# Optimization experiments

Measured on AMD Instinct MI355X. Metric: run time of the kernel, lower is better.

The kernel has to match this reference:

```python
import jax, jax.numpy as jnp
import numpy as np

FP8_MAX = 448.0  # max normal of float8_e4m3fn (TE fwd format)
EPS = 1e-12


def _fp8_quant_dequant(t):
    """Per-tensor amax scaling -> cast to e4m3 -> dequant back to f32.
    Mirrors TE's per-tensor scaling recipe (scale = FP8_MAX / amax)."""
    amax = jnp.max(jnp.abs(t))
    scale = FP8_MAX / jnp.maximum(amax, EPS)
    q = jnp.clip(t * scale, -FP8_MAX, FP8_MAX).astype(jnp.float8_e4m3fn)
    return q.astype(jnp.float32) / scale


def setup_inputs() -> dict:
    key = jax.random.key(0)
    k1, k2, k3 = jax.random.split(key, 3)
    tokens, d_in, d_out = 8192, 4096, 4096
    x = jax.random.normal(k1, (tokens, d_in), dtype=jnp.float32)
    # kaiming_uniform_(a=sqrt(5)) -> U(-bound, bound), bound = sqrt(6/((1+a^2)*fan_in)) = 1/sqrt(fan_in)
    bound = 1.0 / np.sqrt(d_in)
    weight = jax.random.uniform(k2, (d_out, d_in), dtype=jnp.float32, minval=-bound, maxval=bound)
    bias = jnp.zeros((d_out,), dtype=jnp.float32) + 0.01 * jax.random.normal(k3, (d_out,), dtype=jnp.float32)
    return {"x": x, "weight": weight, "bias": bias}


def reference(x, weight, bias):
    # fp8 quant/dequant of activations and weights, then GEMM + bias
    xq = _fp8_quant_dequant(x)            # [T, Din]
    wq = _fp8_quant_dequant(weight)       # [Dout, Din]
    out = jnp.einsum("ti,oi->to", xq, wq) # [T, Dout]
    return out + bias[None, :]
```

## Files before the change

kernel.cpp:

```cpp
#include <hip/hip_runtime.h>
#include <stdint.h>

#define M_DIM 8192
#define N_DIM 4096
#define K_DIM 4096

typedef float f32x4 __attribute__((ext_vector_type(4)));
typedef int   i32x4 __attribute__((ext_vector_type(4)));
typedef int   i32x8 __attribute__((ext_vector_type(8)));

__global__ __launch_bounds__(256) void amax2_kernel(const float* __restrict__ x,
                                                    const float* __restrict__ wgt,
                                                    unsigned int* __restrict__ ws_u) {
    const int which = blockIdx.y;
    const float4* p = (const float4*)(which ? wgt : x);
    const int n4 = (which ? N_DIM : M_DIM) * (K_DIM / 4);
    int tid = blockIdx.x * blockDim.x + threadIdx.x;
    int stride = gridDim.x * blockDim.x;
    float m = 0.0f;
    for (int i = tid; i < n4; i += stride) {
        float4 v = p[i];
        m = fmaxf(m, fmaxf(fmaxf(fabsf(v.x), fabsf(v.y)),
                           fmaxf(fabsf(v.z), fabsf(v.w))));
    }
#pragma unroll
    for (int off = 32; off > 0; off >>= 1)
        m = fmaxf(m, __shfl_down(m, off, 64));
    __shared__ float sm[4];
    if ((threadIdx.x & 63) == 0) sm[threadIdx.x >> 6] = m;
    __syncthreads();
    if (threadIdx.x == 0) {
        m = fmaxf(fmaxf(sm[0], sm[1]), fmaxf(sm[2], sm[3]));
        atomicMax(ws_u + which, __float_as_uint(m));
    }
}

__global__ __launch_bounds__(256) void quant2_kernel(const float* __restrict__ x,
                                                     const float* __restrict__ wgt,
                                                     unsigned int* __restrict__ xq,
                                                     unsigned int* __restrict__ wq,
                                                     const unsigned int* __restrict__ ws_u) {
    const int which = blockIdx.y;
    const float4* p = (const float4*)(which ? wgt : x);
    unsigned int* outp = which ? wq : xq;
    const int n4 = (which ? N_DIM : M_DIM) * (K_DIM / 4);
    float amax = fmaxf(__uint_as_float(ws_u[which]), 1e-12f);
    float scale = 448.0f / amax;
    int tid = blockIdx.x * blockDim.x + threadIdx.x;
    int stride = gridDim.x * blockDim.x;
    for (int i = tid; i < n4; i += stride) {
        float4 v = p[i];
        float a = fminf(fmaxf(v.x * scale, -448.0f), 448.0f);
        float b = fminf(fmaxf(v.y * scale, -448.0f), 448.0f);
        float c = fminf(fmaxf(v.z * scale, -448.0f), 448.0f);
        float d = fminf(fmaxf(v.w * scale, -448.0f), 448.0f);
        int w = __builtin_amdgcn_cvt_pk_fp8_f32(a, b, 0, false);
        w = __builtin_amdgcn_cvt_pk_fp8_f32(c, d, w, true);
        outp[i] = (unsigned int)w;
    }
}

__device__ __forceinline__ void gld16(const void* g, void* l) {
    __builtin_amdgcn_global_load_lds(
        (const __attribute__((address_space(1))) void*)g,
        (__attribute__((address_space(3))) void*)l, 16, 0, 0);
}

__device__ __forceinline__ i32x8 ld2(const uint8_t* bl, const uint8_t* bh, int off) {
    i32x4 lo = *(const i32x4*)(bl + off);
    i32x4 hi = *(const i32x4*)(bh + off);
    return __builtin_shufflevector(lo, hi, 0, 1, 2, 3, 4, 5, 6, 7);
}

#define MFMA_MX(a, b, c) __builtin_amdgcn_mfma_scale_f32_16x16x128_f8f6f4( \
    (a), (b), (c), 0, 0, 0, 0x7F7F7F7F, 0, 0x7F7F7F7F)

__global__ __launch_bounds__(512, 2) void gemm_fp8_kernel(
    const uint8_t* __restrict__ Aq,
    const uint8_t* __restrict__ Bq,
    const float* __restrict__ bias,
    const unsigned int* __restrict__ ws_u,
    float* __restrict__ out)
{
    __shared__ uint8_t lds[131072];

    const int tid = threadIdx.x;
    const int w = tid >> 6, l = tid & 63;

    const int cpx = (int)gridDim.x >> 3;
    const int bid = (int)blockIdx.x;
    const int swz = (bid & 7) * cpx + (bid >> 3);
    const int bm = swz >> 4, bn = swz & 15;

    const uint8_t* gA = Aq + (size_t)bm * 256 * K_DIM;
    const uint8_t* gB = Bq + (size_t)bn * 256 * K_DIM;

    const int idx = tid >> 3, p = tid & 7;
    const int rB = (idx & 31) + ((idx >> 5) << 6);
    const int srcX = ((p ^ (idx & 7)) << 4);
    const int dA = tid * 16;
    const int dB = tid * 16 + ((tid >> 8) << 12);

    const int wr = w >> 2, wc = w & 3;
    const int lr = l & 15, g = l >> 4;
    const int oLo = (((2 * g) ^ (lr & 7)) << 4);
    const int oHi = (((2 * g + 1) ^ (lr & 7)) << 4);
    const int rowA0 = wr * 128 + lr;
    const int rowB0 = wc * 64 + lr;

    const int aOffL = (rowA0 << 7) + oLo, aOffH = (rowA0 << 7) + oHi;
    const int bOffL = (rowB0 << 7) + oLo, bOffH = (rowB0 << 7) + oHi;

    auto stA = [&](int bb, const uint8_t* gsrc, int rbase) {
        const int row = idx + rbase;
        gld16(gsrc + (size_t)row * K_DIM + srcX,
              &lds[bb * 32768 + rbase * 128 + dA]);
    };
    auto stB = [&](int bb, const uint8_t* gsrc, int boff, int r) {
        const int row = rB + boff + (r << 7);
        gld16(gsrc + (size_t)row * K_DIM + srcX,
              &lds[65536 + bb * 32768 + (boff << 7) + (r << 14) + dB]);
    };

    f32x4 acc[8][4] = {};
    i32x8 av[4], bv[4];

    stA(0, gA, 0);   stA(0, gA, 128);
    stB(0, gB, 0, 0); stB(0, gB, 0, 1);
    stA(0, gA, 64);  stA(0, gA, 192);
    stB(0, gB, 32, 0); stB(0, gB, 32, 1);

    for (int t = 0; t < 31; ++t) {
        const int buf = t & 1, nbuf = buf ^ 1;
        const uint8_t* gAn = gA + (size_t)(t + 1) * 128;
        const uint8_t* gBn = gB + (size_t)(t + 1) * 128;
        const uint8_t* qaL = &lds[buf * 32768] + aOffL;
        const uint8_t* qaH = &lds[buf * 32768] + aOffH;
        const uint8_t* qbL = &lds[65536 + buf * 32768] + bOffL;
        const uint8_t* qbH = &lds[65536 + buf * 32768] + bOffH;

        asm volatile("s_waitcnt vmcnt(4)" ::: "memory");
        __builtin_amdgcn_s_barrier();
        stA(nbuf, gAn, 0); stA(nbuf, gAn, 128);
        av[0] = ld2(qaL, qaH, 0);     av[1] = ld2(qaL, qaH, 2048);
        av[2] = ld2(qaL, qaH, 4096);  av[3] = ld2(qaL, qaH, 6144);
        bv[0] = ld2(qbL, qbH, 0);     bv[1] = ld2(qbL, qbH, 2048);
        __builtin_amdgcn_s_setprio(1);
        acc[0][0] = MFMA_MX(av[0], bv[0], acc[0][0]);
        acc[0][1] = MFMA_MX(av[0], bv[1], acc[0][1]);
        acc[1][0] = MFMA_MX(av[1], bv[0], acc[1][0]);
        acc[1][1] = MFMA_MX(av[1], bv[1], acc[1][1]);
        acc[2][0] = MFMA_MX(av[2], bv[0], acc[2][0]);
        acc[2][1] = MFMA_MX(av[2], bv[1], acc[2][1]);
        acc[3][0] = MFMA_MX(av[3], bv[0], acc[3][0]);
        acc[3][1] = MFMA_MX(av[3], bv[1], acc[3][1]);
        __builtin_amdgcn_s_setprio(0);

        asm volatile("s_waitcnt vmcnt(2)" ::: "memory");
        __builtin_amdgcn_s_barrier();
        stB(nbuf, gBn, 0, 0); stB(nbuf, gBn, 0, 1);
        bv[2] = ld2(qbL, qbH, 4096);  bv[3] = ld2(qbL, qbH, 6144);
        __builtin_amdgcn_s_setprio(1);
        acc[0][2] = MFMA_MX(av[0], bv[2], acc[0][2]);
        acc[0][3] = MFMA_MX(av[0], bv[3], acc[0][3]);
        acc[1][2] = MFMA_MX(av[1], bv[2], acc[1][2]);
        acc[1][3] = MFMA_MX(av[1], bv[3], acc[1][3]);
        acc[2][2] = MFMA_MX(av[2], bv[2], acc[2][2]);
        acc[2][3] = MFMA_MX(av[2], bv[3], acc[2][3]);
        acc[3][2] = MFMA_MX(av[3], bv[2], acc[3][2]);
        acc[3][3] = MFMA_MX(av[3], bv[3], acc[3][3]);
        __builtin_amdgcn_s_setprio(0);

        stA(nbuf, gAn, 64); stA(nbuf, gAn, 192);
        av[0] = ld2(qaL, qaH, 8192);  av[1] = ld2(qaL, qaH, 10240);
        av[2] = ld2(qaL, qaH, 12288); av[3] = ld2(qaL, qaH, 14336);
        __builtin_amdgcn_s_setprio(1);
        acc[4][0] = MFMA_MX(av[0], bv[0], acc[4][0]);
        acc[4][1] = MFMA_MX(av[0], bv[1], acc[4][1]);
        acc[5][0] = MFMA_MX(av[1], bv[0], acc[5][0]);
        acc[5][1] = MFMA_MX(av[1], bv[1], acc[5][1]);
        acc[6][0] = MFMA_MX(av[2], bv[0], acc[6][0]);
        acc[6][1] = MFMA_MX(av[2], bv[1], acc[6][1]);
        acc[7][0] = MFMA_MX(av[3], bv[0], acc[7][0]);
        acc[7][1] = MFMA_MX(av[3], bv[1], acc[7][1]);
        __builtin_amdgcn_s_setprio(0);

        stB(nbuf, gBn, 32, 0); stB(nbuf, gBn, 32, 1);
        __builtin_amdgcn_s_setprio(1);
        acc[4][2] = MFMA_MX(av[0], bv[2], acc[4][2]);
        acc[4][3] = MFMA_MX(av[0], bv[3], acc[4][3]);
        acc[5][2] = MFMA_MX(av[1], bv[2], acc[5][2]);
        acc[5][3] = MFMA_MX(av[1], bv[3], acc[5][3]);
        acc[6][2] = MFMA_MX(av[2], bv[2], acc[6][2]);
        acc[6][3] = MFMA_MX(av[2], bv[3], acc[6][3]);
        acc[7][2] = MFMA_MX(av[3], bv[2], acc[7][2]);
        acc[7][3] = MFMA_MX(av[3], bv[3], acc[7][3]);
        __builtin_amdgcn_s_setprio(0);
    }

    {
        const uint8_t* qaL = &lds[32768] + aOffL;
        const uint8_t* qaH = &lds[32768] + aOffH;
        const uint8_t* qbL = &lds[65536 + 32768] + bOffL;
        const uint8_t* qbH = &lds[65536 + 32768] + bOffH;

        asm volatile("s_waitcnt vmcnt(4)" ::: "memory");
        __builtin_amdgcn_s_barrier();
        av[0] = ld2(qaL, qaH, 0);     av[1] = ld2(qaL, qaH, 2048);
        av[2] = ld2(qaL, qaH, 4096);  av[3] = ld2(qaL, qaH, 6144);
        bv[0] = ld2(qbL, qbH, 0);     bv[1] = ld2(qbL, qbH, 2048);
#pragma unroll
        for (int m = 0; m < 4; ++m) {
            acc[m][0] = MFMA_MX(av[m], bv[0], acc[m][0]);
            acc[m][1] = MFMA_MX(av[m], bv[1], acc[m][1]);
        }
        asm volatile("s_waitcnt vmcnt(0)" ::: "memory");
        __builtin_amdgcn_s_barrier();
        bv[2] = ld2(qbL, qbH, 4096);  bv[3] = ld2(qbL, qbH, 6144);
#pragma unroll
        for (int m = 0; m < 4; ++m) {
            acc[m][2] = MFMA_MX(av[m], bv[2], acc[m][2]);
            acc[m][3] = MFMA_MX(av[m], bv[3], acc[m][3]);
        }
        av[0] = ld2(qaL, qaH, 8192);  av[1] = ld2(qaL, qaH, 10240);
        av[2] = ld2(qaL, qaH, 12288); av[3] = ld2(qaL, qaH, 14336);
#pragma unroll
        for (int m = 0; m < 4; ++m) {
            acc[4 + m][0] = MFMA_MX(av[m], bv[0], acc[4 + m][0]);
            acc[4 + m][1] = MFMA_MX(av[m], bv[1], acc[4 + m][1]);
            acc[4 + m][2] = MFMA_MX(av[m], bv[2], acc[4 + m][2]);
            acc[4 + m][3] = MFMA_MX(av[m], bv[3], acc[4 + m][3]);
        }
    }

    const float ax = fmaxf(__uint_as_float(ws_u[0]), 1e-12f);
    const float aw = fmaxf(__uint_as_float(ws_u[1]), 1e-12f);
    const float inv = (ax * (1.0f / 448.0f)) * (aw * (1.0f / 448.0f));

    const int orow0 = bm * 256 + wr * 128 + g * 4;
    const int ocol0 = bn * 256 + wc * 64 + lr;
#pragma unroll
    for (int mb = 0; mb < 8; ++mb) {
#pragma unroll
        for (int nb = 0; nb < 4; ++nb) {
            const int col = ocol0 + nb * 16;
            const float bvv = bias[col];
#pragma unroll
            for (int j = 0; j < 4; ++j) {
                const int row = orow0 + mb * 16 + j;
                out[(size_t)row * N_DIM + col] = acc[mb][nb][j] * inv + bvv;
            }
        }
    }
}

extern "C" void kernel_launch(void* const* d_in, const int* in_sizes, int n_in,
                              void* d_out, int out_size, void* d_ws, size_t ws_size,
                              hipStream_t stream) {
    const float* x    = (const float*)d_in[0];
    const float* wgt  = (const float*)d_in[1];
    const float* bias = (const float*)d_in[2];
    float* out = (float*)d_out;

    unsigned int* ws_u = (unsigned int*)d_ws;
    uint8_t* xq = (uint8_t*)d_ws + 256;
    uint8_t* wq = xq + (size_t)M_DIM * K_DIM;

    hipMemsetAsync(d_ws, 0, 8, stream);

    dim3 ga(1024, 2);
    amax2_kernel<<<ga, 256, 0, stream>>>(x, wgt, ws_u);

    dim3 gq(2048, 2);
    quant2_kernel<<<gq, 256, 0, stream>>>(x, wgt, (unsigned int*)xq,
                                          (unsigned int*)wq, ws_u);

    gemm_fp8_kernel<<<(M_DIM / 256) * (N_DIM / 256), 512, 0, stream>>>(
        xq, wq, bias, ws_u, out);
}
```

Measured before the change: 211.6 us.

## Split GEMM workgroup into dedicated loader waves and MFMA compute waves

```diff
diff --git a/kernel.cpp b/kernel.cpp
--- a/kernel.cpp
+++ b/kernel.cpp
@@ -74,8 +74,12 @@
 
 #define MFMA_MX(a, b, c) __builtin_amdgcn_mfma_scale_f32_16x16x128_f8f6f4( \
     (a), (b), (c), 0, 0, 0, 0x7F7F7F7F, 0, 0x7F7F7F7F)
-
-__global__ __launch_bounds__(512, 2) void gemm_fp8_kernel(
+#define BAR()    __builtin_amdgcn_s_barrier()
+#define VMCNT0() asm volatile("s_waitcnt vmcnt(0)" ::: "memory")
+#define PRIO1()  __builtin_amdgcn_s_setprio(1)
+#define PRIO0()  __builtin_amdgcn_s_setprio(0)
+
+__global__ __launch_bounds__(768, 1) void gemm_fp8_kernel(
     const uint8_t* __restrict__ Aq,
     const uint8_t* __restrict__ Bq,
     const float* __restrict__ bias,
@@ -95,11 +99,41 @@
     const uint8_t* gA = Aq + (size_t)bm * 256 * K_DIM;
     const uint8_t* gB = Bq + (size_t)bn * 256 * K_DIM;
 
-    const int idx = tid >> 3, p = tid & 7;
-    const int rB = (idx & 31) + ((idx >> 5) << 6);
-    const int srcX = ((p ^ (idx & 7)) << 4);
-    const int dA = tid * 16;
-    const int dB = tid * 16 + ((tid >> 8) << 12);
+    if (w >= 8) {
+        const int tid2 = tid - 512;
+        const int idx = tid2 >> 3, p = tid2 & 7;
+        const int srcX = ((p ^ (idx & 7)) << 4);
+        const uint8_t* aRow = gA + (size_t)idx * K_DIM + srcX;
+        const uint8_t* bRow = gB + (size_t)idx * K_DIM + srcX;
+        const int dst = tid2 * 16;
+
+#pragma unroll
+        for (int r = 0; r < 8; ++r)
+            gld16(aRow + (size_t)(r * 32) * K_DIM, &lds[r * 4096 + dst]);
+#pragma unroll
+        for (int r = 0; r < 8; ++r)
+            gld16(bRow + (size_t)(r * 32) * K_DIM, &lds[65536 + r * 4096 + dst]);
+        VMCNT0();
+        BAR();
+
+        for (int t = 0; t < 32; ++t) {
+            if (t < 31) {
+                const int nb = (t + 1) & 1;
+                const int kn = (t + 1) * 128;
+#pragma unroll
+                for (int r = 0; r < 8; ++r)
+                    gld16(aRow + (size_t)(r * 32) * K_DIM + kn,
+                          &lds[nb * 32768 + r * 4096 + dst]);
+#pragma unroll
+                for (int r = 0; r < 8; ++r)
+                    gld16(bRow + (size_t)(r * 32) * K_DIM + kn,
+                          &lds[65536 + nb * 32768 + r * 4096 + dst]);
+                VMCNT0();
+            }
+            BAR();
+        }
+        return;
+    }
 
     const int wr = w >> 2, wc = w & 3;
     const int lr = l & 15, g = l >> 4;
@@ -107,45 +141,25 @@
     const int oHi = (((2 * g + 1) ^ (lr & 7)) << 4);
     const int rowA0 = wr * 128 + lr;
     const int rowB0 = wc * 64 + lr;
-
     const int aOffL = (rowA0 << 7) + oLo, aOffH = (rowA0 << 7) + oHi;
     const int bOffL = (rowB0 << 7) + oLo, bOffH = (rowB0 << 7) + oHi;
 
-    auto stA = [&](int bb, const uint8_t* gsrc, int rbase) {
-        const int row = idx + rbase;
-        gld16(gsrc + (size_t)row * K_DIM + srcX,
-              &lds[bb * 32768 + rbase * 128 + dA]);
-    };
-    auto stB = [&](int bb, const uint8_t* gsrc, int boff, int r) {
-        const int row = rB + boff + (r << 7);
-        gld16(gsrc + (size_t)row * K_DIM + srcX,
-              &lds[65536 + bb * 32768 + (boff << 7) + (r << 14) + dB]);
-    };
-
     f32x4 acc[8][4] = {};
     i32x8 av[4], bv[4];
 
-    stA(0, gA, 0);   stA(0, gA, 128);
-    stB(0, gB, 0, 0); stB(0, gB, 0, 1);
-    stA(0, gA, 64);  stA(0, gA, 192);
-    stB(0, gB, 32, 0); stB(0, gB, 32, 1);
-
-    for (int t = 0; t < 31; ++t) {
-        const int buf = t & 1, nbuf = buf ^ 1;
-        const uint8_t* gAn = gA + (size_t)(t + 1) * 128;
-        const uint8_t* gBn = gB + (size_t)(t + 1) * 128;
+    BAR();
+
+    for (int t = 0; t < 32; ++t) {
+        const int buf = t & 1;
         const uint8_t* qaL = &lds[buf * 32768] + aOffL;
         const uint8_t* qaH = &lds[buf * 32768] + aOffH;
         const uint8_t* qbL = &lds[65536 + buf * 32768] + bOffL;
         const uint8_t* qbH = &lds[65536 + buf * 32768] + bOffH;
 
-        asm volatile("s_waitcnt vmcnt(4)" ::: "memory");
-        __builtin_amdgcn_s_barrier();
-        stA(nbuf, gAn, 0); stA(nbuf, gAn, 128);
         av[0] = ld2(qaL, qaH, 0);     av[1] = ld2(qaL, qaH, 2048);
         av[2] = ld2(qaL, qaH, 4096);  av[3] = ld2(qaL, qaH, 6144);
         bv[0] = ld2(qbL, qbH, 0);     bv[1] = ld2(qbL, qbH, 2048);
-        __builtin_amdgcn_s_setprio(1);
+        PRIO1();
         acc[0][0] = MFMA_MX(av[0], bv[0], acc[0][0]);
         acc[0][1] = MFMA_MX(av[0], bv[1], acc[0][1]);
         acc[1][0] = MFMA_MX(av[1], bv[0], acc[1][0]);
@@ -154,13 +168,10 @@
         acc[2][1] = MFMA_MX(av[2], bv[1], acc[2][1]);
         acc[3][0] = MFMA_MX(av[3], bv[0], acc[3][0]);
         acc[3][1] = MFMA_MX(av[3], bv[1], acc[3][1]);
-        __builtin_amdgcn_s_setprio(0);
-
-        asm volatile("s_waitcnt vmcnt(2)" ::: "memory");
-        __builtin_amdgcn_s_barrier();
-        stB(nbuf, gBn, 0, 0); stB(nbuf, gBn, 0, 1);
+        PRIO0();
+
         bv[2] = ld2(qbL, qbH, 4096);  bv[3] = ld2(qbL, qbH, 6144);
-        __builtin_amdgcn_s_setprio(1);
+        PRIO1();
         acc[0][2] = MFMA_MX(av[0], bv[2], acc[0][2]);
         acc[0][3] = MFMA_MX(av[0], bv[3], acc[0][3]);
         acc[1][2] = MFMA_MX(av[1], bv[2], acc[1][2]);
@@ -169,12 +180,11 @@
         acc[2][3] = MFMA_MX(av[2], bv[3], acc[2][3]);
         acc[3][2] = MFMA_MX(av[3], bv[2], acc[3][2]);
         acc[3][3] = MFMA_MX(av[3], bv[3], acc[3][3]);
-        __builtin_amdgcn_s_setprio(0);
-
-        stA(nbuf, gAn, 64); stA(nbuf, gAn, 192);
+        PRIO0();
+
         av[0] = ld2(qaL, qaH, 8192);  av[1] = ld2(qaL, qaH, 10240);
         av[2] = ld2(qaL, qaH, 12288); av[3] = ld2(qaL, qaH, 14336);
-        __builtin_amdgcn_s_setprio(1);
+        PRIO1();
         acc[4][0] = MFMA_MX(av[0], bv[0], acc[4][0]);
         acc[4][1] = MFMA_MX(av[0], bv[1], acc[4][1]);
         acc[5][0] = MFMA_MX(av[1], bv[0], acc[5][0]);
@@ -183,10 +193,9 @@
         acc[6][1] = MFMA_MX(av[2], bv[1], acc[6][1]);
         acc[7][0] = MFMA_MX(av[3], bv[0], acc[7][0]);
         acc[7][1] = MFMA_MX(av[3], bv[1], acc[7][1]);
-        __builtin_amdgcn_s_setprio(0);
-
-        stB(nbuf, gBn, 32, 0); stB(nbuf, gBn, 32, 1);
-        __builtin_amdgcn_s_setprio(1);
+        PRIO0();
+
+        PRIO1();
         acc[4][2] = MFMA_MX(av[0], bv[2], acc[4][2]);
         acc[4][3] = MFMA_MX(av[0], bv[3], acc[4][3]);
         acc[5][2] = MFMA_MX(av[1], bv[2], acc[5][2]);
@@ -195,42 +204,9 @@
         acc[6][3] = MFMA_MX(av[2], bv[3], acc[6][3]);
         acc[7][2] = MFMA_MX(av[3], bv[2], acc[7][2]);
         acc[7][3] = MFMA_MX(av[3], bv[3], acc[7][3]);
-        __builtin_amdgcn_s_setprio(0);
-    }
-
-    {
-        const uint8_t* qaL = &lds[32768] + aOffL;
-        const uint8_t* qaH = &lds[32768] + aOffH;
-        const uint8_t* qbL = &lds[65536 + 32768] + bOffL;
-        const uint8_t* qbH = &lds[65536 + 32768] + bOffH;
-
-        asm volatile("s_waitcnt vmcnt(4)" ::: "memory");
-        __builtin_amdgcn_s_barrier();
-        av[0] = ld2(qaL, qaH, 0);     av[1] = ld2(qaL, qaH, 2048);
-        av[2] = ld2(qaL, qaH, 4096);  av[3] = ld2(qaL, qaH, 6144);
-        bv[0] = ld2(qbL, qbH, 0);     bv[1] = ld2(qbL, qbH, 2048);
-#pragma unroll
-        for (int m = 0; m < 4; ++m) {
-            acc[m][0] = MFMA_MX(av[m], bv[0], acc[m][0]);
-            acc[m][1] = MFMA_MX(av[m], bv[1], acc[m][1]);
-        }
-        asm volatile("s_waitcnt vmcnt(0)" ::: "memory");
-        __builtin_amdgcn_s_barrier();
-        bv[2] = ld2(qbL, qbH, 4096);  bv[3] = ld2(qbL, qbH, 6144);
-#pragma unroll
-        for (int m = 0; m < 4; ++m) {
-            acc[m][2] = MFMA_MX(av[m], bv[2], acc[m][2]);
-            acc[m][3] = MFMA_MX(av[m], bv[3], acc[m][3]);
-        }
-        av[0] = ld2(qaL, qaH, 8192);  av[1] = ld2(qaL, qaH, 10240);
-        av[2] = ld2(qaL, qaH, 12288); av[3] = ld2(qaL, qaH, 14336);
-#pragma unroll
-        for (int m = 0; m < 4; ++m) {
-            acc[4 + m][0] = MFMA_MX(av[m], bv[0], acc[4 + m][0]);
-            acc[4 + m][1] = MFMA_MX(av[m], bv[1], acc[4 + m][1]);
-            acc[4 + m][2] = MFMA_MX(av[m], bv[2], acc[4 + m][2]);
-            acc[4 + m][3] = MFMA_MX(av[m], bv[3], acc[4 + m][3]);
-        }
+        PRIO0();
+
+        BAR();
     }
 
     const float ax = fmaxf(__uint_as_float(ws_u[0]), 1e-12f);
@@ -275,6 +251,6 @@
     quant2_kernel<<<gq, 256, 0, stream>>>(x, wgt, (unsigned int*)xq,
                                           (unsigned int*)wq, ws_u);
 
-    gemm_fp8_kernel<<<(M_DIM / 256) * (N_DIM / 256), 512, 0, stream>>>(
+    gemm_fp8_kernel<<<(M_DIM / 256) * (N_DIM / 256), 768, 0, stream>>>(
         xq, wq, bias, ws_u, out);
 }
```

Result: slower. 666.6 us (+215.1%).
